# Performance work log

Hardware: AMD Instinct MI355X
Metric: run time of the kernel (lower is better)

Reference implementation:

```python
import jax, jax.numpy as jnp
import numpy as np
from jax import lax

GRID = 50
T_DIM = 1
Y_DIM = GRID * GRID
R_DIM = 128
Z_DIM = 64
H_DIM = 128
C_CONV = 32


def _conv(x, w, b):
    # x: [N, Cin, H, W], w: [Cout, Cin, 3, 3]
    y = lax.conv_general_dilated(x, w, (1, 1), 'SAME',
                                 dimension_numbers=('NCHW', 'OIHW', 'NCHW'))
    return y + b[None, :, None, None]


def setup_inputs() -> dict:
    key = jax.random.key(0)
    ks = jax.random.split(key, 24)
    B, NC, NT = 16, 64, 128
    s = lambda k, sh, f: (jax.random.normal(k, sh, jnp.float32) * f)
    inp = {
        'x_context': jax.random.normal(ks[0], (B, NC, T_DIM), jnp.float32),
        'y_context': jax.random.normal(ks[1], (B, NC, Y_DIM), jnp.float32),
        'x_target': jax.random.normal(ks[2], (B, NT, T_DIM), jnp.float32),
        'eps': jax.random.normal(ks[3], (B, Z_DIM), jnp.float32),
        # CNN encoder (Net)
        'w1': s(ks[4], (C_CONV, 2, 3, 3), 0.2), 'b1': jnp.zeros((C_CONV,), jnp.float32),
        'w2': s(ks[5], (C_CONV, C_CONV, 3, 3), 0.1), 'b2': jnp.zeros((C_CONV,), jnp.float32),
        'We1': s(ks[6], (C_CONV + T_DIM, H_DIM), 0.1), 'be1': jnp.zeros((H_DIM,), jnp.float32),
        'We2': s(ks[7], (H_DIM, R_DIM), 0.1), 'be2': jnp.zeros((R_DIM,), jnp.float32),
        # MuSigmaEncoder
        'Wh': s(ks[8], (R_DIM, H_DIM), 0.1), 'bh': jnp.zeros((H_DIM,), jnp.float32),
        'Wmu': s(ks[9], (H_DIM, Z_DIM), 0.1), 'bmu': jnp.zeros((Z_DIM,), jnp.float32),
        'Wsig': s(ks[10], (H_DIM, Z_DIM), 0.1), 'bsig': jnp.zeros((Z_DIM,), jnp.float32),
        # Decoder
        'Wd1': s(ks[11], (T_DIM + Z_DIM, H_DIM), 0.1), 'bd1': jnp.zeros((H_DIM,), jnp.float32),
        'Wd2': s(ks[12], (H_DIM, H_DIM), 0.1), 'bd2': jnp.zeros((H_DIM,), jnp.float32),
        'Wdmu': s(ks[13], (H_DIM, Y_DIM), 0.05), 'bdmu': jnp.zeros((Y_DIM,), jnp.float32),
        'Wdsig': s(ks[14], (H_DIM, Y_DIM), 0.05), 'bdsig': jnp.zeros((Y_DIM,), jnp.float32),
    }
    return inp


def _xy_to_mu_sigma(x, y, p):
    B, N, _ = x.shape
    x_flat = x.reshape(B * N, T_DIM)                      # [BN, 1]
    y_grid = y.reshape(B * N, 1, GRID, GRID)              # [BN,1,50,50]
    # broadcast of x value over the grid (replaces per-sample Python loop)
    x_grid = jnp.broadcast_to(x_flat[:, 0, None, None, None], (B * N, 1, GRID, GRID))
    xy_grid = jnp.concatenate([y_grid, x_grid], axis=1)   # [BN,2,50,50]
    h = jax.nn.relu(_conv(xy_grid, p['w1'], p['b1']))
    h = jax.nn.relu(_conv(h, p['w2'], p['b2']))
    pooled = h.mean(axis=(2, 3))                          # [BN, C_CONV]
    feat = jnp.concatenate([pooled, x_flat], axis=-1)     # [BN, C_CONV+1]
    r_i = jnp.dot(jax.nn.relu(jnp.dot(feat, p['We1']) + p['be1']), p['We2']) + p['be2']
    r = r_i.reshape(B, N, R_DIM).mean(axis=1)             # aggregate over points
    hr = jax.nn.relu(jnp.dot(r, p['Wh']) + p['bh'])
    mu = jnp.dot(hr, p['Wmu']) + p['bmu']
    sigma = 0.1 + 0.9 * jax.nn.sigmoid(jnp.dot(hr, p['Wsig']) + p['bsig'])
    return mu, sigma


def _decode(x_target, z, p):
    B, M, _ = x_target.shape
    z_rep = jnp.broadcast_to(z[:, None, :], (B, M, Z_DIM))
    xz = jnp.concatenate([x_target, z_rep], axis=-1)      # [B,M,1+Z]
    h = jax.nn.relu(jnp.dot(xz, p['Wd1']) + p['bd1'])
    h = jax.nn.relu(jnp.dot(h, p['Wd2']) + p['bd2'])
    y_mu = jnp.dot(h, p['Wdmu']) + p['bdmu']
    y_sigma = 0.1 + 0.9 * jax.nn.softplus(jnp.dot(h, p['Wdsig']) + p['bdsig'])
    return y_mu, y_sigma


def reference(x_context, y_context, x_target, eps,
              w1, b1, w2, b2, We1, be1, We2, be2,
              Wh, bh, Wmu, bmu, Wsig, bsig,
              Wd1, bd1, Wd2, bd2, Wdmu, bdmu, Wdsig, bdsig):
    p = dict(w1=w1, b1=b1, w2=w2, b2=b2, We1=We1, be1=be1, We2=We2, be2=be2,
             Wh=Wh, bh=bh, Wmu=Wmu, bmu=bmu, Wsig=Wsig, bsig=bsig,
             Wd1=Wd1, bd1=bd1, Wd2=Wd2, bd2=bd2, Wdmu=Wdmu, bdmu=bdmu,
             Wdsig=Wdsig, bdsig=bdsig)
    mu_c, sigma_c = _xy_to_mu_sigma(x_context, y_context, p)
    z = mu_c + sigma_c * eps                               # rsample (reparameterized)
    y_mu, y_sigma = _decode(x_target, z, p)
    return y_mu, y_sigma, mu_c, sigma_c
```

## Files before the change

### kernel.cpp

```cpp
#include <hip/hip_runtime.h>

#define GRID_N   50
#define YDIM     2500
#define BATCH    16
#define NCTX     64
#define NTGT     128
#define BN       1024
#define RDIM     128
#define ZDIM     64
#define HDIM     128
#define CCONV    32
#define NSTRIP   5
#define STRIPROWS 10

typedef __attribute__((ext_vector_type(8))) short  s8v;
typedef __attribute__((ext_vector_type(4))) float  f4v;
typedef __attribute__((ext_vector_type(4))) unsigned int u4v;

__device__ __forceinline__ unsigned short f2bf(float f) {
    unsigned int u = __float_as_uint(f);
    u += 0x7FFFu + ((u >> 16) & 1u);
    return (unsigned short)(u >> 16);
}
__device__ __forceinline__ unsigned int cvtpk(float lo, float hi) {
    unsigned int r;
    asm("v_cvt_pk_bf16_f32 %0, %1, %2" : "=v"(r) : "v"(lo), "v"(hi));
    return r;
}


#define PLB   31024
#define PY    2
#define PX    738
#define P1    1490
#define DUP   2228
#define SMEMB 39936


__global__ void k_pack(const float* __restrict__ w1, const float* __restrict__ b1,
                       const float* __restrict__ w2,
                       unsigned short* __restrict__ w2p, unsigned short* __restrict__ w1p,
                       const float* __restrict__ Wmu, const float* __restrict__ Wsg,
                       unsigned short* __restrict__ wdp)
{
    int t = threadIdx.x;
    if (blockIdx.y == 2) {
        if (blockIdx.x != 0) return;
        int l = t & 63, qq = t >> 6;
        int cout_lo = l & 15, cb = (l >> 4) & 3;
        for (int e = qq; e < 18; e += 4) {
            int tap = e >> 1, ntt = e & 1;
            int cout = ntt * 16 + cout_lo;
            unsigned int pk[4];
#pragma unroll
            for (int g = 0; g < 4; ++g) {
                int jj = 2 * g;
                int cinL = (jj < 4) ? (cb * 4 + jj) : (16 + cb * 4 + (jj - 4));
                unsigned int lo = f2bf(w2[(cout * 32 + cinL) * 9 + tap]);
                unsigned int hi = f2bf(w2[(cout * 32 + cinL + 1) * 9 + tap]);
                pk[g] = lo | (hi << 16);
            }
            uint4 o; o.x = pk[0]; o.y = pk[1]; o.z = pk[2]; o.w = pk[3];
            *(uint4*)&w2p[((tap * 2 + ntt) * 64 + l) * 8] = o;
        }
        if (t < 128) {
            int ct = t >> 6, lane = t & 63;
            int c = ct * 16 + (lane & 15), q2 = lane >> 4;
            const signed char kmap[32] = {0,1,3,4,6,7,16,17,  2,-1,5,-1,8,-1,18,-1,
                                          19,20,21,-1,22,23,24,-1, 32,-1,-1,-1,-1,-1,-1,-1};
            unsigned short v8[8];
#pragma unroll
            for (int j = 0; j < 8; ++j) {
                int km = kmap[q2 * 8 + j];
                float v = 0.f;
                if (km == 32) v = b1[c];
                else if (km >= 16) v = w1[(c * 2 + 1) * 9 + (km - 16)];
                else if (km >= 0) v = w1[(c * 2 + 0) * 9 + km];
                v8[j] = f2bf(v);
            }
            uint4 o;
            o.x = (unsigned)v8[0] | ((unsigned)v8[1] << 16);
            o.y = (unsigned)v8[2] | ((unsigned)v8[3] << 16);
            o.z = (unsigned)v8[4] | ((unsigned)v8[5] << 16);
            o.w = (unsigned)v8[6] | ((unsigned)v8[7] << 16);
            *(uint4*)&w1p[(ct * 64 + lane) * 8] = o;
        }
        return;
    }
    int nt = blockIdx.x;
    int which = blockIdx.y;
    const float* W = which ? Wsg : Wmu;
    unsigned short* outp = wdp + (size_t)which * (157 * 4 * 64 * 8);
    int l = t & 63, ks = t >> 6;
    int n = nt * 16 + (l & 15);
    int kbase = ks * 32 + ((l >> 4) & 3) * 8;
    unsigned int pk[4];
#pragma unroll
    for (int g = 0; g < 4; ++g) {
        float f0 = (n < 2500) ? W[(kbase + 2 * g) * 2500 + n] : 0.f;
        float f1 = (n < 2500) ? W[(kbase + 2 * g + 1) * 2500 + n] : 0.f;
        pk[g] = (unsigned int)f2bf(f0) | ((unsigned int)f2bf(f1) << 16);
    }
    uint4 o; o.x = pk[0]; o.y = pk[1]; o.z = pk[2]; o.w = pk[3];
    *(uint4*)&outp[((nt * 4 + ks) * 64 + l) * 8] = o;
}

__global__ __launch_bounds__(256, 4) void k_conv(
    const float* __restrict__ xc, const float* __restrict__ yc,
    const unsigned short* __restrict__ w1p, const unsigned short* __restrict__ w2p,
    const float* __restrict__ b2, float* __restrict__ part)
{
    __shared__ __align__(16) char smem[SMEMB];
    unsigned short* pl = (unsigned short*)(smem + PLB);
    float* redbuf = (float*)smem;

    const int t = threadIdx.x, lane = t & 63, w = t >> 6;
    const int l15 = lane & 15, q = lane >> 4;
    const int par = lane & 1;
    const int blk = blockIdx.x, s = blk / NSTRIP, strip = blk - s * NSTRIP;
    const int r0 = strip * STRIPROWS;

    const float xv = xc[s];
    const unsigned short xbf = f2bf(xv);
    const float b2v0 = b2[l15], b2v1 = b2[16 + l15];

    for (int e = t; e < 736; e += 256) {
        unsigned ry = ((unsigned)(e * 1261)) >> 16;
        int ycol = e - (int)ry * 52;
        int gy = r0 - 2 + (int)ry, gc = ycol - 1;
        bool inb = ((unsigned)gy < 50u) && ((unsigned)gc < 50u);
        unsigned short yb = 0, xb = 0;
        if (inb) { yb = f2bf(yc[s * YDIM + gy * 50 + gc]); xb = xbf; }
        int s0 = PY + e, s1 = PX + e, s2 = P1 + e;
        pl[s0] = yb; if (s0 >= 3) pl[DUP + s0 - 3] = yb;
        pl[s1] = xb; pl[DUP + s1 - 3] = xb;
        pl[s2] = 0x3F80; pl[DUP + s2 - 3] = 0x3F80;
    }

    s8v w1f[2];
#pragma unroll
    for (int ct = 0; ct < 2; ++ct)
        w1f[ct] = *(const s8v*)&w1p[(ct * 64 + lane) * 8];

    int B0 = (q == 0) ? 1 : (q == 1) ? 3 : (q == 2) ? 789 : P1;
    int B1 = (q < 2) ? (B0 + 52)  : ((q == 2) ? 791 : P1);
    int B2 = (q < 2) ? (B0 + 104) : ((q == 2) ? 841 : P1);
    int B3 = (q < 2) ? (B0 + 736) : ((q == 2) ? 843 : P1);
    auto mkoff = [&](int B) {
        int pr = (B + lane) & 1;
        return PLB + ((pr ? (DUP - 3 + B) : B) << 1);
    };
    const int bo0 = mkoff(B0), bo1 = mkoff(B1), bo2 = mkoff(B2), bo3 = mkoff(B3);

    __syncthreads();

    const f4v zf = {0.f, 0.f, 0.f, 0.f};
    auto do_tile = [&](int mt) -> uint4 {
        int m = mt * 16 + l15;
        int mb = m * 2;
        unsigned g0 = *(const unsigned*)(smem + bo0 + mb);
        unsigned g1 = *(const unsigned*)(smem + bo1 + mb);
        unsigned g2 = *(const unsigned*)(smem + bo2 + mb);
        unsigned g3 = *(const unsigned*)(smem + bo3 + mb);
        u4v gg = {g0, g1, g2, g3};
        s8v af = __builtin_bit_cast(s8v, gg);
        f4v c0 = __builtin_amdgcn_mfma_f32_16x16x32_bf16(w1f[0], af, zf, 0, 0, 0);
        f4v c1 = __builtin_amdgcn_mfma_f32_16x16x32_bf16(w1f[1], af, zf, 0, 0, 0);
        unsigned mr = ((unsigned)(m * 1261)) >> 16;
        int mc = m - (int)mr * 52;
        int gy = r0 - 1 + (int)mr;
        bool valid = ((unsigned)(mc - 1) < 50u) && ((unsigned)gy < 50u);
        unsigned p0 = cvtpk(fmaxf(c0[0], 0.f), fmaxf(c0[1], 0.f));
        unsigned p1 = cvtpk(fmaxf(c0[2], 0.f), fmaxf(c0[3], 0.f));
        unsigned p2 = cvtpk(fmaxf(c1[0], 0.f), fmaxf(c1[1], 0.f));
        unsigned p3 = cvtpk(fmaxf(c1[2], 0.f), fmaxf(c1[3], 0.f));
        if (!valid) { p0 = 0u; p1 = 0u; p2 = 0u; p3 = 0u; }
        return make_uint4(p0, p1, p2, p3);
    };
    auto wr_tile = [&](int mt, uint4 v) {
        int m = mt * 16 + l15;
        int rrow = m >> 1;
        int slot = (((m & 1) << 2) | q) ^ (rrow & 7);
        *(uint4*)(smem + (rrow << 7) + (slot << 4)) = v;
    };

#pragma unroll
    for (int it = 0; it < 8; ++it) {
        int mt = w + it * 4;
        if (mt <= 29) {
            uint4 v = do_tile(mt);
            wr_tile(mt, v);
        }
    }
    {
        int mt0 = (w >= 2) ? (28 + w) : (32 + w);
        uint4 hA = do_tile(mt0);
        uint4 hB = do_tile(mt0 + 4);
        uint4 hC = make_uint4(0u, 0u, 0u, 0u);
        bool third = (w == 2);
        if (third) hC = do_tile(38);
        __syncthreads();
        wr_tile(mt0, hA);
        wr_tile(mt0 + 4, hB);
        if (third) wr_tile(38, hC);
    }
    __syncthreads();

    f4v acc[8][2];
#pragma unroll
    for (int i = 0; i < 8; ++i) { acc[i][0] = zf; acc[i][1] = zf; }
    int u_[8], up_[8];
#pragma unroll
    for (int tt = 0; tt < 8; ++tt) {
        int m2 = (w * 8 + tt) * 16 + l15;
        unsigned orr = ((unsigned)(m2 * 1311)) >> 16;
        int pc = m2 + 2 * (int)orr;
        int u = pc >> 1;
        u = (u > 258) ? 258 : u;
        u_[tt] = u;
        up_[tt] = u + par;
    }
    const int oq  = (par << 2) | q;
    const int oqx = ((par ^ 1) << 2) | q;
    __builtin_amdgcn_s_setprio(1);
#pragma unroll
    for (int tp = 0; tp < 9; ++tp) {
        const int ky = tp / 3, kx = tp % 3;
        s8v b0 = *(const s8v*)&w2p[((tp * 2 + 0) * 64 + lane) * 8];
        s8v b1 = *(const s8v*)&w2p[((tp * 2 + 1) * 64 + lane) * 8];
#pragma unroll
        for (int tt = 0; tt < 8; ++tt) {
            int r = (kx == 1 ? up_[tt] : u_[tt]) + 26 * ky + (kx == 2 ? 1 : 0);
            int so = ((kx == 1 ? oqx : oq) ^ (r & 7)) << 4;
            s8v a = *(const s8v*)(smem + (r << 7) + so);
            acc[tt][0] = __builtin_amdgcn_mfma_f32_16x16x32_bf16(a, b0, acc[tt][0], 0, 0, 0);
            acc[tt][1] = __builtin_amdgcn_mfma_f32_16x16x32_bf16(a, b1, acc[tt][1], 0, 0, 0);
        }
    }
    __builtin_amdgcn_s_setprio(0);

    float ps0 = 0.f, ps1 = 0.f;
#pragma unroll
    for (int tt = 0; tt < 8; ++tt) {
        int tile = w * 8 + tt;
        if (tile != 31) {
#pragma unroll
            for (int r = 0; r < 4; ++r) {
                ps0 += fmaxf(acc[tt][0][r] + b2v0, 0.f);
                ps1 += fmaxf(acc[tt][1][r] + b2v1, 0.f);
            }
        } else {
            int mbase = tile * 16 + q * 4;
#pragma unroll
            for (int r = 0; r < 4; ++r) {
                if (mbase + r < 500) {
                    ps0 += fmaxf(acc[tt][0][r] + b2v0, 0.f);
                    ps1 += fmaxf(acc[tt][1][r] + b2v1, 0.f);
                }
            }
        }
    }
    ps0 += __shfl_xor(ps0, 16); ps0 += __shfl_xor(ps0, 32);
    ps1 += __shfl_xor(ps1, 16); ps1 += __shfl_xor(ps1, 32);
    __syncthreads();
    if (lane < 16) {
        redbuf[w * 32 + l15] = ps0;
        redbuf[w * 32 + 16 + l15] = ps1;
    }
    __syncthreads();
    if (t < 32)
        part[(s * NSTRIP + strip) * 32 + t] =
            redbuf[t] + redbuf[32 + t] + redbuf[64 + t] + redbuf[96 + t];
}

__global__ void k_enc(const float* __restrict__ part, const float* __restrict__ xc,
                      const float* __restrict__ We1, const float* __restrict__ be1,
                      const float* __restrict__ We2, const float* __restrict__ be2,
                      float* __restrict__ r_i)
{
    __shared__ float feat[33];
    __shared__ float h[128];
    int s = blockIdx.x, j = threadIdx.x;
    if (j < 32) {
        float v = 0.f;
#pragma unroll
        for (int st = 0; st < NSTRIP; ++st) v += part[(s * NSTRIP + st) * 32 + j];
        feat[j] = v * (1.f / 2500.f);
    }
    if (j == 0) feat[32] = xc[s];
    __syncthreads();
    float a = be1[j];
#pragma unroll 4
    for (int k = 0; k < 33; ++k) a = fmaf(feat[k], We1[k * 128 + j], a);
    h[j] = fmaxf(a, 0.f);
    __syncthreads();
    float r = be2[j];
#pragma unroll 8
    for (int k = 0; k < 128; ++k) r = fmaf(h[k], We2[k * 128 + j], r);
    r_i[s * 128 + j] = r;
}

__global__ void k_ms(const float* __restrict__ r_i,
                     const float* __restrict__ Wh, const float* __restrict__ bh,
                     const float* __restrict__ Wmu, const float* __restrict__ bmu,
                     const float* __restrict__ Wsig, const float* __restrict__ bsig,
                     const float* __restrict__ eps, float* __restrict__ out,
                     float* __restrict__ zbuf)
{
    __shared__ float r[128], hr[128], tmp[2][128];
    int b = blockIdx.x, t = threadIdx.x;
    int j = t & 127, g = t >> 7;
    float acc = 0.f;
#pragma unroll 4
    for (int i = g; i < NCTX; i += 2) acc += r_i[(b * NCTX + i) * 128 + j];
    tmp[g][j] = acc;
    __syncthreads();
    if (g == 0) r[j] = (tmp[0][j] + tmp[1][j]) * (1.f / 64.f);
    __syncthreads();
    float a = (g == 0) ? bh[j] : 0.f;
#pragma unroll 8
    for (int k = g * 64; k < g * 64 + 64; ++k) a = fmaf(r[k], Wh[k * 128 + j], a);
    tmp[g][j] = a;
    __syncthreads();
    if (g == 0) hr[j] = fmaxf(tmp[0][j] + tmp[1][j], 0.f);
    __syncthreads();
    if (j < 64) {
        float m = (g == 0) ? bmu[j] : 0.f, sg = (g == 0) ? bsig[j] : 0.f;
#pragma unroll 8
        for (int k = g * 64; k < g * 64 + 64; ++k) {
            m  = fmaf(hr[k], Wmu[k * 64 + j], m);
            sg = fmaf(hr[k], Wsig[k * 64 + j], sg);
        }
        tmp[g][j] = m; tmp[g][64 + j] = sg;
    }
    __syncthreads();
    if (t < 64) {
        float m  = tmp[0][t] + tmp[1][t];
        float sg = tmp[0][64 + t] + tmp[1][64 + t];
        float sig = 0.1f + 0.9f / (1.f + expf(-sg));
        out[10240000 + b * 64 + t] = m;
        out[10241024 + b * 64 + t] = sig;
        zbuf[b * 64 + t] = m + sig * eps[b * 64 + t];
    }
}

__global__ __launch_bounds__(256) void k_dec1(
    const float* __restrict__ xt, const float* __restrict__ zbuf,
    const float* __restrict__ Wd1, const float* __restrict__ bd1,
    const float* __restrict__ Wd2, const float* __restrict__ bd2,
    unsigned short* __restrict__ h2d)
{
    __shared__ float zsh[64];
    __shared__ float vsh[2][128];
    __shared__ float h1sh[4][128];
    int t = threadIdx.x;
    int j = t & 127, g = t >> 7;
    int r0 = blockIdx.x * 4;
    int b = r0 >> 7;
    if (t < 64) zsh[t] = zbuf[b * 64 + t];
    __syncthreads();
    float v = (g == 0) ? bd1[j] : 0.f;
#pragma unroll 8
    for (int k = g * 32; k < g * 32 + 32; ++k)
        v = fmaf(zsh[k], Wd1[(1 + k) * 128 + j], v);
    vsh[g][j] = v;
    __syncthreads();
    float vv = vsh[0][j] + vsh[1][j];
    float w0 = Wd1[j];
    int ra = r0 + g * 2;
    float x0 = xt[ra], x1 = xt[ra + 1];
    h1sh[g * 2][j]     = fmaxf(fmaf(x0, w0, vv), 0.f);
    h1sh[g * 2 + 1][j] = fmaxf(fmaf(x1, w0, vv), 0.f);
    __syncthreads();
    float bd2j = bd2[j];
    float a0 = bd2j, a1 = bd2j;
#pragma unroll 8
    for (int k = 0; k < 128; ++k) {
        float wv = Wd2[k * 128 + j];
        a0 = fmaf(h1sh[g * 2][k], wv, a0);
        a1 = fmaf(h1sh[g * 2 + 1][k], wv, a1);
    }
    h2d[(size_t)ra * 128 + j]       = f2bf(fmaxf(a0, 0.f));
    h2d[(size_t)(ra + 1) * 128 + j] = f2bf(fmaxf(a1, 0.f));
}

__global__ __launch_bounds__(256) void k_gemm(
    const unsigned short* __restrict__ h2d, const unsigned short* __restrict__ wdp,
    const float* __restrict__ bdmu, const float* __restrict__ bdsg,
    float* __restrict__ out)
{
    __shared__ __align__(16) unsigned short Al[64 * 128];
    int t = threadIdx.x, lane = t & 63, w = t >> 6;
    int m0 = blockIdx.x * 64;
#pragma unroll
    for (int i = 0; i < 4; ++i) {
        int g = t + i * 256;
        int row = g >> 4, bk = g & 15;
        uint4 v = *(const uint4*)&h2d[(size_t)(m0 + row) * 128 + bk * 8];
        *(uint4*)&Al[row * 128 + ((bk ^ (row & 7)) << 3)] = v;
    }
    __syncthreads();
    int nt = blockIdx.y * 4 + w;
    if (nt < 157) {
        int lcol = lane & 15, lq = lane >> 4;
        int col = nt * 16 + lcol;
#pragma unroll
        for (int which = 0; which < 2; ++which) {
            const unsigned short* wp = wdp + (size_t)which * (157 * 4 * 64 * 8);
            s8v bfr[4];
#pragma unroll
            for (int ks = 0; ks < 4; ++ks)
                bfr[ks] = *(const s8v*)&wp[((nt * 4 + ks) * 64 + lane) * 8];
            f4v acc[4];
            {
                f4v zf = {0.f, 0.f, 0.f, 0.f};
#pragma unroll
                for (int mt = 0; mt < 4; ++mt) acc[mt] = zf;
            }
#pragma unroll
            for (int mt = 0; mt < 4; ++mt) {
                int mrow = mt * 16 + lcol;
#pragma unroll
                for (int ks = 0; ks < 4; ++ks) {
                    int bk = ks * 4 + lq;
                    s8v a = *(const s8v*)&Al[mrow * 128 + ((bk ^ (mrow & 7)) << 3)];
                    acc[mt] = __builtin_amdgcn_mfma_f32_16x16x32_bf16(a, bfr[ks], acc[mt], 0, 0, 0);
                }
            }
            if (col < 2500) {
                const float* bp = which ? bdsg : bdmu;
                float bv = bp[col];
                size_t zoff = (size_t)which * 5120000;
#pragma unroll
                for (int mt = 0; mt < 4; ++mt)
#pragma unroll
                    for (int r = 0; r < 4; ++r) {
                        int row = m0 + mt * 16 + lq * 4 + r;
                        float vv = acc[mt][r] + bv;
                        if (which) {
                            float sp = fmaxf(vv, 0.f) + log1pf(expf(-fabsf(vv)));
                            vv = 0.1f + 0.9f * sp;
                        }
                        out[zoff + (size_t)row * 2500 + col] = vv;
                    }
            }
        }
    }
}

extern "C" void kernel_launch(void* const* d_in, const int* in_sizes, int n_in,
                              void* d_out, int out_size, void* d_ws, size_t ws_size,
                              hipStream_t stream)
{
    const float* xc   = (const float*)d_in[0];
    const float* yc   = (const float*)d_in[1];
    const float* xt   = (const float*)d_in[2];
    const float* eps  = (const float*)d_in[3];
    const float* w1   = (const float*)d_in[4];
    const float* b1   = (const float*)d_in[5];
    const float* w2   = (const float*)d_in[6];
    const float* b2   = (const float*)d_in[7];
    const float* We1  = (const float*)d_in[8];
    const float* be1  = (const float*)d_in[9];
    const float* We2  = (const float*)d_in[10];
    const float* be2  = (const float*)d_in[11];
    const float* Wh   = (const float*)d_in[12];
    const float* bh   = (const float*)d_in[13];
    const float* Wmu  = (const float*)d_in[14];
    const float* bmu  = (const float*)d_in[15];
    const float* Wsig = (const float*)d_in[16];
    const float* bsig = (const float*)d_in[17];
    const float* Wd1  = (const float*)d_in[18];
    const float* bd1  = (const float*)d_in[19];
    const float* Wd2  = (const float*)d_in[20];
    const float* bd2  = (const float*)d_in[21];
    const float* Wdmu = (const float*)d_in[22];
    const float* bdmu = (const float*)d_in[23];
    const float* Wdsg = (const float*)d_in[24];
    const float* bdsg = (const float*)d_in[25];

    float* out = (float*)d_out;
    char* wsb  = (char*)d_ws;
    unsigned short* w2p = (unsigned short*)(wsb + 0);
    unsigned short* wdp = (unsigned short*)(wsb + 18432);
    float* part = (float*)(wsb + 1304576);
    float* r_i  = (float*)(wsb + 1959936);
    float* zbuf = (float*)(wsb + 2484224);
    unsigned short* h2d = (unsigned short*)(wsb + 2488320);
    unsigned short* w1p = (unsigned short*)(wsb + 3012608);

    hipLaunchKernelGGL(k_pack, dim3(157, 3), dim3(256), 0, stream,
                       w1, b1, w2, w2p, w1p, Wdmu, Wdsg, wdp);
    hipLaunchKernelGGL(k_conv, dim3(BN * NSTRIP), dim3(256), 0, stream,
                       xc, yc, w1p, w2p, b2, part);
    hipLaunchKernelGGL(k_enc, dim3(BN), dim3(128), 0, stream,
                       part, xc, We1, be1, We2, be2, r_i);
    hipLaunchKernelGGL(k_ms, dim3(BATCH), dim3(256), 0, stream,
                       r_i, Wh, bh, Wmu, bmu, Wsig, bsig, eps, out, zbuf);
    hipLaunchKernelGGL(k_dec1, dim3(512), dim3(256), 0, stream,
                       xt, zbuf, Wd1, bd1, Wd2, bd2, h2d);
    hipLaunchKernelGGL(k_gemm, dim3(32, 40), dim3(256), 0, stream,
                       h2d, wdp, bdmu, bdsg, out);
}
```

Measured before the change: 118.1 us.

## Fold constant x channel of conv1 into per-region bias and double conv block size

The x-channel of the first convolution is constant per sample, so its contribution is precomputed in the pack kernel as nine boundary-region weight sums (tregG) and added as xv*tregG plus bias after the MFMA. This shrinks the staged plane to only y values and cuts the A-fragment loads from four to two. The conv kernel also moves to 512 threads (8 waves) with half the tiles per wave, trading more per-block parallelism for occupancy and register pressure changes. The result is exact except for bf16 rounding of the x term, which now stays in fp32.

```diff
diff --git a/kernel.cpp b/kernel.cpp
--- a/kernel.cpp
+++ b/kernel.cpp
@@ -29,17 +29,14 @@
 }
 
 
-#define PLB   31024
-#define PY    2
-#define PX    738
-#define P1    1490
-#define DUP   2228
+#define PLB   35840
 #define SMEMB 39936
 
 
 __global__ void k_pack(const float* __restrict__ w1, const float* __restrict__ b1,
                        const float* __restrict__ w2,
                        unsigned short* __restrict__ w2p, unsigned short* __restrict__ w1p,
+                       float* __restrict__ tregG,
                        const float* __restrict__ Wmu, const float* __restrict__ Wsg,
                        unsigned short* __restrict__ wdp)
 {
@@ -66,17 +63,15 @@
         if (t < 128) {
             int ct = t >> 6, lane = t & 63;
             int c = ct * 16 + (lane & 15), q2 = lane >> 4;
-            const signed char kmap[32] = {0,1,3,4,6,7,16,17,  2,-1,5,-1,8,-1,18,-1,
-                                          19,20,21,-1,22,23,24,-1, 32,-1,-1,-1,-1,-1,-1,-1};
+            const signed char ktab[16] = {0,1,3,4,  6,7,2,-1,  5,-1,8,-1,  -1,-1,-1,-1};
             unsigned short v8[8];
 #pragma unroll
             for (int j = 0; j < 8; ++j) {
-                int km = kmap[q2 * 8 + j];
-                float v = 0.f;
-                if (km == 32) v = b1[c];
-                else if (km >= 16) v = w1[(c * 2 + 1) * 9 + (km - 16)];
-                else if (km >= 0) v = w1[(c * 2 + 0) * 9 + km];
-                v8[j] = f2bf(v);
+                v8[j] = 0;
+                if (j < 4) {
+                    int km = ktab[q2 * 4 + j];
+                    if (km >= 0) v8[j] = f2bf(w1[(c * 2 + 0) * 9 + km]);
+                }
             }
             uint4 o;
             o.x = (unsigned)v8[0] | ((unsigned)v8[1] << 16);
@@ -84,6 +79,18 @@
             o.z = (unsigned)v8[4] | ((unsigned)v8[5] << 16);
             o.w = (unsigned)v8[6] | ((unsigned)v8[7] << 16);
             *(uint4*)&w1p[(ct * 64 + lane) * 8] = o;
+        }
+        for (int e = t; e < 288; e += 256) {
+            int ridx = e >> 5, c = e & 31;
+            int rr = ridx / 3, cc = ridx % 3;
+            float sum = 0.f;
+            for (int ky = 0; ky < 3; ++ky)
+                for (int kx = 0; kx < 3; ++kx) {
+                    bool rok = !((rr == 0 && ky == 0) || (rr == 2 && ky == 2));
+                    bool cok = !((cc == 0 && kx == 0) || (cc == 2 && kx == 2));
+                    if (rok && cok) sum += w1[(c * 2 + 1) * 9 + ky * 3 + kx];
+                }
+            tregG[e] = sum;
         }
         return;
     }
@@ -105,10 +112,11 @@
     *(uint4*)&outp[((nt * 4 + ks) * 64 + l) * 8] = o;
 }
 
-__global__ __launch_bounds__(256, 4) void k_conv(
+__global__ __launch_bounds__(512, 8) void k_conv(
     const float* __restrict__ xc, const float* __restrict__ yc,
     const unsigned short* __restrict__ w1p, const unsigned short* __restrict__ w2p,
-    const float* __restrict__ b2, float* __restrict__ part)
+    const float* __restrict__ b1, const float* __restrict__ b2,
+    const float* __restrict__ tregG, float* __restrict__ part)
 {
     __shared__ __align__(16) char smem[SMEMB];
     unsigned short* pl = (unsigned short*)(smem + PLB);
@@ -121,20 +129,20 @@
     const int r0 = strip * STRIPROWS;
 
     const float xv = xc[s];
-    const unsigned short xbf = f2bf(xv);
     const float b2v0 = b2[l15], b2v1 = b2[16 + l15];
-
-    for (int e = t; e < 736; e += 256) {
+    const float4 bv0 = *(const float4*)&b1[q * 4];
+    const float4 bv1 = *(const float4*)&b1[16 + q * 4];
+
+    if (t == 0) pl[0] = 0;
+    for (int e = t; e < 736; e += 512) {
         unsigned ry = ((unsigned)(e * 1261)) >> 16;
         int ycol = e - (int)ry * 52;
         int gy = r0 - 2 + (int)ry, gc = ycol - 1;
-        bool inb = ((unsigned)gy < 50u) && ((unsigned)gc < 50u);
-        unsigned short yb = 0, xb = 0;
-        if (inb) { yb = f2bf(yc[s * YDIM + gy * 50 + gc]); xb = xbf; }
-        int s0 = PY + e, s1 = PX + e, s2 = P1 + e;
-        pl[s0] = yb; if (s0 >= 3) pl[DUP + s0 - 3] = yb;
-        pl[s1] = xb; pl[DUP + s1 - 3] = xb;
-        pl[s2] = 0x3F80; pl[DUP + s2 - 3] = 0x3F80;
+        unsigned short yb = 0;
+        if (((unsigned)gy < 50u) && ((unsigned)gc < 50u))
+            yb = f2bf(yc[s * YDIM + gy * 50 + gc]);
+        pl[1 + e] = yb;
+        if (e < 734) pl[738 + e] = yb;
     }
 
     s8v w1f[2];
@@ -142,15 +150,13 @@
     for (int ct = 0; ct < 2; ++ct)
         w1f[ct] = *(const s8v*)&w1p[(ct * 64 + lane) * 8];
 
-    int B0 = (q == 0) ? 1 : (q == 1) ? 3 : (q == 2) ? 789 : P1;
-    int B1 = (q < 2) ? (B0 + 52)  : ((q == 2) ? 791 : P1);
-    int B2 = (q < 2) ? (B0 + 104) : ((q == 2) ? 841 : P1);
-    int B3 = (q < 2) ? (B0 + 736) : ((q == 2) ? 843 : P1);
+    int Ba = (q == 0) ? -1 : (q == 1) ? 103 : (q == 2) ? 53 : -1;
+    int Bb = (q == 0) ? 51 : (q == 1) ? 1 : (q == 2) ? 105 : -1;
     auto mkoff = [&](int B) {
-        int pr = (B + lane) & 1;
-        return PLB + ((pr ? (DUP - 3 + B) : B) << 1);
+        int pr = (B + 1 + par) & 1;
+        return PLB + (pr ? 2 * (738 + B) : 2 * (1 + B));
     };
-    const int bo0 = mkoff(B0), bo1 = mkoff(B1), bo2 = mkoff(B2), bo3 = mkoff(B3);
+    const int bo0 = mkoff(Ba), bo1 = mkoff(Bb);
 
     __syncthreads();
 
@@ -160,16 +166,28 @@
         int mb = m * 2;
         unsigned g0 = *(const unsigned*)(smem + bo0 + mb);
         unsigned g1 = *(const unsigned*)(smem + bo1 + mb);
-        unsigned g2 = *(const unsigned*)(smem + bo2 + mb);
-        unsigned g3 = *(const unsigned*)(smem + bo3 + mb);
-        u4v gg = {g0, g1, g2, g3};
+        u4v gg = {g0, g1, 0u, 0u};
         s8v af = __builtin_bit_cast(s8v, gg);
         f4v c0 = __builtin_amdgcn_mfma_f32_16x16x32_bf16(w1f[0], af, zf, 0, 0, 0);
         f4v c1 = __builtin_amdgcn_mfma_f32_16x16x32_bf16(w1f[1], af, zf, 0, 0, 0);
         unsigned mr = ((unsigned)(m * 1261)) >> 16;
         int mc = m - (int)mr * 52;
         int gy = r0 - 1 + (int)mr;
-        bool valid = ((unsigned)(mc - 1) < 50u) && ((unsigned)gy < 50u);
+        int gc = mc - 1;
+        bool valid = ((unsigned)gc < 50u) && ((unsigned)gy < 50u);
+        int rr = (gy == 0) ? 0 : ((gy == 49) ? 2 : 1);
+        int cc = (gc == 0) ? 0 : ((gc == 49) ? 2 : 1);
+        int ridx = rr * 3 + cc;
+        float4 tg0 = *(const float4*)&tregG[ridx * 32 + q * 4];
+        float4 tg1 = *(const float4*)&tregG[ridx * 32 + 16 + q * 4];
+        c0[0] = fmaf(xv, tg0.x, c0[0] + bv0.x);
+        c0[1] = fmaf(xv, tg0.y, c0[1] + bv0.y);
+        c0[2] = fmaf(xv, tg0.z, c0[2] + bv0.z);
+        c0[3] = fmaf(xv, tg0.w, c0[3] + bv0.w);
+        c1[0] = fmaf(xv, tg1.x, c1[0] + bv1.x);
+        c1[1] = fmaf(xv, tg1.y, c1[1] + bv1.y);
+        c1[2] = fmaf(xv, tg1.z, c1[2] + bv1.z);
+        c1[3] = fmaf(xv, tg1.w, c1[3] + bv1.w);
         unsigned p0 = cvtpk(fmaxf(c0[0], 0.f), fmaxf(c0[1], 0.f));
         unsigned p1 = cvtpk(fmaxf(c0[2], 0.f), fmaxf(c0[3], 0.f));
         unsigned p2 = cvtpk(fmaxf(c1[0], 0.f), fmaxf(c1[1], 0.f));
@@ -184,41 +202,34 @@
         *(uint4*)(smem + (rrow << 7) + (slot << 4)) = v;
     };
 
-#pragma unroll
-    for (int it = 0; it < 8; ++it) {
-        int mt = w + it * 4;
-        if (mt <= 29) {
+#pragma unroll 5
+    for (int it = 0; it < 5; ++it) {
+        int mt = w + it * 8;
+        if (mt <= 34) {
             uint4 v = do_tile(mt);
             wr_tile(mt, v);
         }
     }
     {
-        int mt0 = (w >= 2) ? (28 + w) : (32 + w);
-        uint4 hA = do_tile(mt0);
-        uint4 hB = do_tile(mt0 + 4);
-        uint4 hC = make_uint4(0u, 0u, 0u, 0u);
-        bool third = (w == 2);
-        if (third) hC = do_tile(38);
+        bool hold = (w < 4);
+        uint4 hA = make_uint4(0u, 0u, 0u, 0u);
+        int mt0 = 35 + w;
+        if (hold) hA = do_tile(mt0);
         __syncthreads();
-        wr_tile(mt0, hA);
-        wr_tile(mt0 + 4, hB);
-        if (third) wr_tile(38, hC);
-    }
-    __syncthreads();
-
-    f4v acc[8][2];
-#pragma unroll
-    for (int i = 0; i < 8; ++i) { acc[i][0] = zf; acc[i][1] = zf; }
-    int u_[8], up_[8];
-#pragma unroll
-    for (int tt = 0; tt < 8; ++tt) {
-        int m2 = (w * 8 + tt) * 16 + l15;
+        if (hold) wr_tile(mt0, hA);
+    }
+    __syncthreads();
+
+    f4v acc[4][2];
+#pragma unroll
+    for (int i = 0; i < 4; ++i) { acc[i][0] = zf; acc[i][1] = zf; }
+    int u_[4];
+#pragma unroll
+    for (int tt = 0; tt < 4; ++tt) {
+        int m2 = (w * 4 + tt) * 16 + l15;
         unsigned orr = ((unsigned)(m2 * 1311)) >> 16;
-        int pc = m2 + 2 * (int)orr;
-        int u = pc >> 1;
-        u = (u > 258) ? 258 : u;
-        u_[tt] = u;
-        up_[tt] = u + par;
+        int u = (m2 + 2 * (int)orr) >> 1;
+        u_[tt] = (u > 258) ? 258 : u;
     }
     const int oq  = (par << 2) | q;
     const int oqx = ((par ^ 1) << 2) | q;
@@ -227,22 +238,22 @@
     for (int tp = 0; tp < 9; ++tp) {
         const int ky = tp / 3, kx = tp % 3;
         s8v b0 = *(const s8v*)&w2p[((tp * 2 + 0) * 64 + lane) * 8];
-        s8v b1 = *(const s8v*)&w2p[((tp * 2 + 1) * 64 + lane) * 8];
-#pragma unroll
-        for (int tt = 0; tt < 8; ++tt) {
-            int r = (kx == 1 ? up_[tt] : u_[tt]) + 26 * ky + (kx == 2 ? 1 : 0);
+        s8v b1f = *(const s8v*)&w2p[((tp * 2 + 1) * 64 + lane) * 8];
+#pragma unroll
+        for (int tt = 0; tt < 4; ++tt) {
+            int r = u_[tt] + 26 * ky + ((kx == 1) ? par : (kx == 2 ? 1 : 0));
             int so = ((kx == 1 ? oqx : oq) ^ (r & 7)) << 4;
             s8v a = *(const s8v*)(smem + (r << 7) + so);
             acc[tt][0] = __builtin_amdgcn_mfma_f32_16x16x32_bf16(a, b0, acc[tt][0], 0, 0, 0);
-            acc[tt][1] = __builtin_amdgcn_mfma_f32_16x16x32_bf16(a, b1, acc[tt][1], 0, 0, 0);
+            acc[tt][1] = __builtin_amdgcn_mfma_f32_16x16x32_bf16(a, b1f, acc[tt][1], 0, 0, 0);
         }
     }
     __builtin_amdgcn_s_setprio(0);
 
     float ps0 = 0.f, ps1 = 0.f;
 #pragma unroll
-    for (int tt = 0; tt < 8; ++tt) {
-        int tile = w * 8 + tt;
+    for (int tt = 0; tt < 4; ++tt) {
+        int tile = w * 4 + tt;
         if (tile != 31) {
 #pragma unroll
             for (int r = 0; r < 4; ++r) {
@@ -268,9 +279,12 @@
         redbuf[w * 32 + 16 + l15] = ps1;
     }
     __syncthreads();
-    if (t < 32)
-        part[(s * NSTRIP + strip) * 32 + t] =
-            redbuf[t] + redbuf[32 + t] + redbuf[64 + t] + redbuf[96 + t];
+    if (t < 32) {
+        float v = 0.f;
+#pragma unroll
+        for (int k = 0; k < 8; ++k) v += redbuf[k * 32 + t];
+        part[(s * NSTRIP + strip) * 32 + t] = v;
+    }
 }
 
 __global__ void k_enc(const float* __restrict__ part, const float* __restrict__ xc,
@@ -488,11 +502,12 @@
     float* zbuf = (float*)(wsb + 2484224);
     unsigned short* h2d = (unsigned short*)(wsb + 2488320);
     unsigned short* w1p = (unsigned short*)(wsb + 3012608);
+    float* treg = (float*)(wsb + 3014656);
 
     hipLaunchKernelGGL(k_pack, dim3(157, 3), dim3(256), 0, stream,
-                       w1, b1, w2, w2p, w1p, Wdmu, Wdsg, wdp);
-    hipLaunchKernelGGL(k_conv, dim3(BN * NSTRIP), dim3(256), 0, stream,
-                       xc, yc, w1p, w2p, b2, part);
+                       w1, b1, w2, w2p, w1p, treg, Wdmu, Wdsg, wdp);
+    hipLaunchKernelGGL(k_conv, dim3(BN * NSTRIP), dim3(512), 0, stream,
+                       xc, yc, w1p, w2p, b1, b2, treg, part);
     hipLaunchKernelGGL(k_enc, dim3(BN), dim3(128), 0, stream,
                        part, xc, We1, be1, We2, be2, r_i);
     hipLaunchKernelGGL(k_ms, dim3(BATCH), dim3(256), 0, stream,
```

After: 121.3 us. +2.8%, slower.
